# Kernel optimization log

Hardware: AMD Instinct MI355X
Metric: run time of the kernel (lower is better)

The kernel has to match this reference:

```python
import jax, jax.numpy as jnp
import numpy as np

N_USERS, N_RECIPES = 100000, 50000
E, L = 600000, 200000
D_USER, D_RECIPE, H, OUT = 128, 256, 128, 64


def _glorot(key, shape):
    fan_in = shape[-1]
    return jax.random.normal(key, shape, dtype=jnp.float32) / np.sqrt(fan_in)


def setup_inputs() -> dict:
    key = jax.random.key(0)
    ks = jax.random.split(key, 24)
    inp = {
        "x_user": jax.random.normal(ks[0], (N_USERS, D_USER), dtype=jnp.float32),
        "x_recipe": jax.random.normal(ks[1], (N_RECIPES, D_RECIPE), dtype=jnp.float32),
        "edge_src": jax.random.randint(ks[2], (E,), 0, N_USERS, dtype=jnp.int32),
        "edge_dst": jax.random.randint(ks[3], (E,), 0, N_RECIPES, dtype=jnp.int32),
        "lbl_src": jax.random.randint(ks[4], (L,), 0, N_USERS, dtype=jnp.int32),
        "lbl_dst": jax.random.randint(ks[5], (L,), 0, N_RECIPES, dtype=jnp.int32),
        # input projections
        "Wu": _glorot(ks[6], (H, D_USER)), "bu": jnp.zeros((H,), jnp.float32),
        "Wrec": _glorot(ks[7], (H, D_RECIPE)), "brec": jnp.zeros((H,), jnp.float32),
        # conv1: user->recipe and recipe->user SAGEConv (lin_l has bias, lin_r no bias)
        "c1_ur_Wl": _glorot(ks[8], (H, H)), "c1_ur_bl": jnp.zeros((H,), jnp.float32),
        "c1_ur_Wr": _glorot(ks[9], (H, H)),
        "c1_ru_Wl": _glorot(ks[10], (H, H)), "c1_ru_bl": jnp.zeros((H,), jnp.float32),
        "c1_ru_Wr": _glorot(ks[11], (H, H)),
        # conv2
        "c2_ur_Wl": _glorot(ks[12], (OUT, H)), "c2_ur_bl": jnp.zeros((OUT,), jnp.float32),
        "c2_ur_Wr": _glorot(ks[13], (OUT, H)),
        "c2_ru_Wl": _glorot(ks[14], (OUT, H)), "c2_ru_bl": jnp.zeros((OUT,), jnp.float32),
        "c2_ru_Wr": _glorot(ks[15], (OUT, H)),
    }
    return inp


def _sage(x_src, x_dst, src_idx, dst_idx, n_dst, Wl, bl, Wr):
    # gather neighbor features, scatter-mean by destination, then linear + root
    msg = x_src[src_idx]                                    # [E, H]
    agg = jax.ops.segment_sum(msg, dst_idx, num_segments=n_dst)
    cnt = jax.ops.segment_sum(jnp.ones((src_idx.shape[0],), x_src.dtype),
                              dst_idx, num_segments=n_dst)
    mean = agg / jnp.maximum(cnt, 1.0)[:, None]             # nodes w/o edges -> 0
    return mean @ Wl.T + bl + x_dst @ Wr.T


def _forward(x_user, x_recipe, Wu, bu, Wrec, brec,
             c1_ur_Wl, c1_ur_bl, c1_ur_Wr, c1_ru_Wl, c1_ru_bl, c1_ru_Wr,
             c2_ur_Wl, c2_ur_bl, c2_ur_Wr, c2_ru_Wl, c2_ru_bl, c2_ru_Wr,
             edge_src, edge_dst, lbl_src, lbl_dst):
    hu = x_user @ Wu.T + bu           # [N_users, H]
    hr = x_recipe @ Wrec.T + brec     # [N_recipes, H]
    # conv1 (user->recipe updates recipe, recipe->user updates user)
    r1 = jax.nn.relu(_sage(hu, hr, edge_src, edge_dst, hr.shape[0], c1_ur_Wl, c1_ur_bl, c1_ur_Wr))
    u1 = jax.nn.relu(_sage(hr, hu, edge_dst, edge_src, hu.shape[0], c1_ru_Wl, c1_ru_bl, c1_ru_Wr))
    # conv2 (dropout is identity in eval mode)
    zr = _sage(u1, r1, edge_src, edge_dst, r1.shape[0], c2_ur_Wl, c2_ur_bl, c2_ur_Wr)
    zu = _sage(r1, u1, edge_dst, edge_src, u1.shape[0], c2_ru_Wl, c2_ru_bl, c2_ru_Wr)
    # decoder: normalized dot product on labeled user-recipe pairs
    zs = zu[lbl_src]
    zd = zr[lbl_dst]
    zs = zs / jnp.maximum(jnp.linalg.norm(zs, axis=1, keepdims=True), 1e-12)
    zd = zd / jnp.maximum(jnp.linalg.norm(zd, axis=1, keepdims=True), 1e-12)
    return jnp.sum(zs * zd, axis=1)   # [L]


def reference(x_user, x_recipe, edge_src, edge_dst, lbl_src, lbl_dst,
              Wu, bu, Wrec, brec,
              c1_ur_Wl, c1_ur_bl, c1_ur_Wr, c1_ru_Wl, c1_ru_bl, c1_ru_Wr,
              c2_ur_Wl, c2_ur_bl, c2_ur_Wr, c2_ru_Wl, c2_ru_bl, c2_ru_Wr):
    return _forward(x_user, x_recipe, Wu, bu, Wrec, brec,
                    c1_ur_Wl, c1_ur_bl, c1_ur_Wr, c1_ru_Wl, c1_ru_bl, c1_ru_Wr,
                    c2_ur_Wl, c2_ur_bl, c2_ur_Wr, c2_ru_Wl, c2_ru_bl, c2_ru_Wr,
                    edge_src, edge_dst, lbl_src, lbl_dst)
```

## Files before the change

### kernel.cpp

```cpp
#include <hip/hip_runtime.h>
#include <hip/hip_bf16.h>
#include <math.h>

#define N_USERS   100000
#define N_RECIPES 50000
#define NE        600000
#define NL        200000
#define DU        128
#define DR        256
#define H         128
#define OUT_D     64

#define NBKT 256
#define NB_R 196
#define NB_U 391

using half2v = __attribute__((ext_vector_type(2))) _Float16;
using half4v = __attribute__((ext_vector_type(4))) _Float16;
using half8v = __attribute__((ext_vector_type(8))) _Float16;
using f32x4  = __attribute__((ext_vector_type(4))) float;

__device__ __forceinline__ int wave_incl_scan(int v, int lane) {
#pragma unroll
  for (int o = 1; o < 64; o <<= 1) {
    int t = __shfl_up(v, o, 64);
    if (lane >= o) v += t;
  }
  return v;
}

struct WPack {
  const float* src[10];
  _Float16* dst[10];
  int sz4[10];
  int* btot;
};
__global__ void convert_weights(WPack p) {
  const int m = blockIdx.y;
  const int i = blockIdx.x * 256 + threadIdx.x;
  if (m == 0 && blockIdx.x == 0) {
    p.btot[threadIdx.x] = 0;
    p.btot[threadIdx.x + 256] = 0;
  }
  if (i < p.sz4[m]) {
    float4 v = ((const float4*)p.src[m])[i];
    half4v h;
    h[0] = (_Float16)v.x; h[1] = (_Float16)v.y;
    h[2] = (_Float16)v.z; h[3] = (_Float16)v.w;
    ((half4v*)p.dst[m])[i] = h;
  }
}

__global__ __launch_bounds__(256) void csr_phase0(const int* __restrict__ esrc,
                                                  const int* __restrict__ edst,
                                                  int* __restrict__ btot) {
  __shared__ int h[512];
  const int tid = threadIdx.x;
  h[tid] = 0; h[tid + 256] = 0;
  __syncthreads();
  for (int i = blockIdx.x * 256 + tid; i < NE; i += gridDim.x * 256) {
    atomicAdd(&h[edst[i] / NB_R], 1);
    atomicAdd(&h[256 + esrc[i] / NB_U], 1);
  }
  __syncthreads();
  if (h[tid]) atomicAdd(&btot[tid], h[tid]);
  if (h[tid + 256]) atomicAdd(&btot[tid + 256], h[tid + 256]);
}

__global__ void csr_bscan(const int* __restrict__ btot,
                          int* __restrict__ bbase_r, int* __restrict__ bcur_r,
                          int* __restrict__ off_r,
                          int* __restrict__ bbase_u, int* __restrict__ bcur_u,
                          int* __restrict__ off_u) {
  __shared__ int wsum[4];
  const int tid = threadIdx.x, lane = tid & 63, wid = tid >> 6;
#pragma unroll
  for (int dir = 0; dir < 2; ++dir) {
    int v = btot[dir * 256 + tid];
    int inc = wave_incl_scan(v, lane);
    if (lane == 63) wsum[wid] = inc;
    __syncthreads();
    int woff = 0;
#pragma unroll
    for (int w = 0; w < 4; ++w)
      if (w < wid) woff += wsum[w];
    int excl = woff + inc - v;
    int* bbase = dir ? bbase_u : bbase_r;
    int* bcur = dir ? bcur_u : bcur_r;
    bbase[tid] = excl;
    bcur[tid] = excl;
    if (tid == 255) bbase[256] = excl + v;
    __syncthreads();
  }
  if (tid == 0) {
    off_r[N_RECIPES] = NE;
    off_u[N_USERS] = NE;
  }
}

__global__ __launch_bounds__(256) void csr_phase1(
    const int* __restrict__ esrc, const int* __restrict__ edst,
    int* __restrict__ bcur_r, int* __restrict__ bcur_u,
    unsigned* __restrict__ stage_r, unsigned* __restrict__ stage_u) {
  __shared__ int cnt[512];
  __shared__ int gbase[512];
  constexpr int EPT = 8;
  const int BATCH = 256 * EPT;
  const int tid = threadIdx.x;
  for (int base = blockIdx.x * BATCH; base < NE; base += gridDim.x * BATCH) {
    cnt[tid] = 0; cnt[tid + 256] = 0;
    __syncthreads();
    int s_[EPT], d_[EPT], rr_[EPT], ru_[EPT];
#pragma unroll
    for (int e = 0; e < EPT; ++e) {
      const int i = base + e * 256 + tid;
      if (i < NE) {
        const int s = esrc[i], d = edst[i];
        s_[e] = s; d_[e] = d;
        rr_[e] = atomicAdd(&cnt[d / NB_R], 1);
        ru_[e] = atomicAdd(&cnt[256 + s / NB_U], 1);
      } else {
        d_[e] = -1;
      }
    }
    __syncthreads();
    if (cnt[tid]) gbase[tid] = atomicAdd(&bcur_r[tid], cnt[tid]);
    if (cnt[tid + 256]) gbase[tid + 256] = atomicAdd(&bcur_u[tid], cnt[tid + 256]);
    __syncthreads();
#pragma unroll
    for (int e = 0; e < EPT; ++e) {
      if (d_[e] >= 0) {
        const int br = d_[e] / NB_R, lr = d_[e] - br * NB_R;
        stage_r[gbase[br] + rr_[e]] = ((unsigned)lr << 17) | (unsigned)s_[e];
        const int bu = s_[e] / NB_U, lu = s_[e] - bu * NB_U;
        stage_u[gbase[256 + bu] + ru_[e]] = ((unsigned)lu << 17) | (unsigned)d_[e];
      }
    }
    __syncthreads();
  }
}

template <int Nv, int NBv>
__device__ __forceinline__ void phase2_impl(int* cnt, int* wsum,
                                            const unsigned* __restrict__ stage,
                                            const int* __restrict__ bbase,
                                            int* __restrict__ offx,
                                            int* __restrict__ eidx, int B) {
  const int tid = threadIdx.x, lane = tid & 63, wid = tid >> 6;
  const int n0 = B * NBv;
  const int nloc = min(NBv, Nv - n0);
  cnt[tid] = 0; cnt[tid + 256] = 0;
  __syncthreads();
  const int s = bbase[B], e = bbase[B + 1];
  for (int i = s + tid; i < e; i += 256)
    atomicAdd(&cnt[stage[i] >> 17], 1);
  __syncthreads();
  const int e0 = cnt[2 * tid], e1 = cnt[2 * tid + 1];
  const int ssum = e0 + e1;
  int inc = wave_incl_scan(ssum, lane);
  if (lane == 63) wsum[wid] = inc;
  __syncthreads();
  int woff = 0;
#pragma unroll
  for (int w = 0; w < 4; ++w)
    if (w < wid) woff += wsum[w];
  const int base = s + woff + inc - ssum;
  if (2 * tid < nloc) offx[n0 + 2 * tid] = base;
  if (2 * tid + 1 < nloc) offx[n0 + 2 * tid + 1] = base + e0;
  cnt[2 * tid] = base;
  cnt[2 * tid + 1] = base + e0;
  __syncthreads();
  for (int i = s + tid; i < e; i += 256) {
    const unsigned p = stage[i];
    const int pos = atomicAdd(&cnt[p >> 17], 1);
    eidx[pos] = (int)(p & 0x1FFFFu);
  }
}

__global__ __launch_bounds__(256) void csr_phase2(
    const unsigned* __restrict__ stage_r, const int* __restrict__ bbase_r,
    int* __restrict__ off_r, int* __restrict__ eidx_r,
    const unsigned* __restrict__ stage_u, const int* __restrict__ bbase_u,
    int* __restrict__ off_u, int* __restrict__ eidx_u) {
  __shared__ int cnt[512];
  __shared__ int wsum[4];
  if (blockIdx.x < NBKT)
    phase2_impl<N_RECIPES, NB_R>(cnt, wsum, stage_r, bbase_r, off_r, eidx_r, blockIdx.x);
  else
    phase2_impl<N_USERS, NB_U>(cnt, wsum, stage_u, bbase_u, off_u, eidx_u, blockIdx.x - NBKT);
}

template <int ROWH, bool ADD, bool DORELU>
__global__ __launch_bounds__(256) void agg_mean2(
    const _Float16* __restrict__ feat, const int* __restrict__ offx,
    const int* __restrict__ eidx, _Float16* __restrict__ outm, int n_dst) {
  constexpr int L = ROWH / 8;
  const int nid = (int)((blockIdx.x * 256 + threadIdx.x) / L);
  const int ln = threadIdx.x & (L - 1);
  if (nid >= n_dst) return;
  const int s = offx[nid], e = offx[nid + 1];
  float a0[8] = {0}, a1[8] = {0}, a2[8] = {0}, a3[8] = {0};
  int i = s;
  for (; i + 3 < e; i += 4) {
    const int r0 = eidx[i], r1 = eidx[i + 1], r2 = eidx[i + 2], r3 = eidx[i + 3];
    half8v v0 = ((const half8v*)(feat + (size_t)r0 * ROWH))[ln];
    half8v v1 = ((const half8v*)(feat + (size_t)r1 * ROWH))[ln];
    half8v v2 = ((const half8v*)(feat + (size_t)r2 * ROWH))[ln];
    half8v v3 = ((const half8v*)(feat + (size_t)r3 * ROWH))[ln];
#pragma unroll
    for (int t = 0; t < 8; ++t) {
      a0[t] += (float)v0[t];
      a1[t] += (float)v1[t];
      a2[t] += (float)v2[t];
      a3[t] += (float)v3[t];
    }
  }
  for (; i < e; ++i) {
    const int r0 = eidx[i];
    half8v v0 = ((const half8v*)(feat + (size_t)r0 * ROWH))[ln];
#pragma unroll
    for (int t = 0; t < 8; ++t) a0[t] += (float)v0[t];
  }
  const float invc = (e > s) ? 1.f / (float)(e - s) : 0.f;
  half8v o, old;
  if (ADD) old = ((const half8v*)(outm + (size_t)nid * ROWH))[ln];
#pragma unroll
  for (int t = 0; t < 8; ++t) {
    float m = (a0[t] + a1[t] + a2[t] + a3[t]) * invc;
    if (ADD) m += (float)old[t];
    if (DORELU) m = fmaxf(m, 0.f);
    o[t] = (_Float16)m;
  }
  ((half8v*)(outm + (size_t)nid * ROWH))[ln] = o;
}

__global__ __launch_bounds__(256) void agg_mean_dual64(
    const _Float16* __restrict__ fA, const int* __restrict__ offA,
    const int* __restrict__ eA, _Float16* __restrict__ oA,
    const _Float16* __restrict__ fB, const int* __restrict__ offB,
    const int* __restrict__ eB, _Float16* __restrict__ oB) {
  const int gnid = (int)((blockIdx.x * 256 + threadIdx.x) >> 3);
  const int ln = threadIdx.x & 7;
  if (gnid >= N_RECIPES + N_USERS) return;
  const _Float16* feat;
  const int* offx;
  const int* eidx;
  _Float16* outm;
  int nid;
  if (gnid < N_RECIPES) {
    feat = fA; offx = offA; eidx = eA; outm = oA; nid = gnid;
  } else {
    feat = fB; offx = offB; eidx = eB; outm = oB; nid = gnid - N_RECIPES;
  }
  const int s = offx[nid], e = offx[nid + 1];
  float a0[8] = {0}, a1[8] = {0}, a2[8] = {0}, a3[8] = {0};
  int i = s;
  for (; i + 3 < e; i += 4) {
    const int r0 = eidx[i], r1 = eidx[i + 1], r2 = eidx[i + 2], r3 = eidx[i + 3];
    half8v v0 = ((const half8v*)(feat + (size_t)r0 * OUT_D))[ln];
    half8v v1 = ((const half8v*)(feat + (size_t)r1 * OUT_D))[ln];
    half8v v2 = ((const half8v*)(feat + (size_t)r2 * OUT_D))[ln];
    half8v v3 = ((const half8v*)(feat + (size_t)r3 * OUT_D))[ln];
#pragma unroll
    for (int t = 0; t < 8; ++t) {
      a0[t] += (float)v0[t];
      a1[t] += (float)v1[t];
      a2[t] += (float)v2[t];
      a3[t] += (float)v3[t];
    }
  }
  for (; i < e; ++i) {
    const int r0 = eidx[i];
    half8v v0 = ((const half8v*)(feat + (size_t)r0 * OUT_D))[ln];
#pragma unroll
    for (int t = 0; t < 8; ++t) a0[t] += (float)v0[t];
  }
  const float invc = (e > s) ? 1.f / (float)(e - s) : 0.f;
  half8v old = ((const half8v*)(outm + (size_t)nid * OUT_D))[ln];
  half8v o;
#pragma unroll
  for (int t = 0; t < 8; ++t)
    o[t] = (_Float16)((a0[t] + a1[t] + a2[t] + a3[t]) * invc + (float)old[t]);
  ((half8v*)(outm + (size_t)nid * OUT_D))[ln] = o;
}

template <int BN, int K, bool DUAL, bool BIAS, bool RELU, bool A_F32>
__global__ __launch_bounds__(256) void gemm_direct(
    const void* __restrict__ A1v, const _Float16* __restrict__ W1,
    const void* __restrict__ A2v, const _Float16* __restrict__ W2,
    const float* __restrict__ bias, _Float16* __restrict__ outp, int M) {
  constexpr int WN = BN / 64;
  constexpr int BM = (4 / WN) * 64;
  const int lane = threadIdx.x & 63;
  const int wid = threadIdx.x >> 6;
  const int wm = wid / WN;
  const int wn = wid % WN;
  const int m0 = blockIdx.x * BM;
  const int lm = lane & 15;
  const int lkb = (lane >> 4) * 8;

  f32x4 acc[4][4];
  const f32x4 zero4 = {0.f, 0.f, 0.f, 0.f};
#pragma unroll
  for (int i = 0; i < 4; ++i)
#pragma unroll
    for (int j = 0; j < 4; ++j) acc[i][j] = zero4;

  int arow[4];
#pragma unroll
  for (int i = 0; i < 4; ++i) {
    int r = m0 + wm * 64 + i * 16 + lm;
    arow[i] = (r < M) ? r : (M - 1);
  }

#pragma unroll
  for (int pass = 0; pass < (DUAL ? 2 : 1); ++pass) {
    const void* Av = pass ? A2v : A1v;
    const _Float16* __restrict__ W = pass ? W2 : W1;
#pragma unroll
    for (int k0 = 0; k0 < K; k0 += 32) {
      half8v af[4], bf[4];
      if constexpr (A_F32) {
        const float* __restrict__ A = (const float*)Av;
#pragma unroll
        for (int i = 0; i < 4; ++i) {
          const float* p = A + (size_t)arow[i] * K + k0 + lkb;
          float4 u = *(const float4*)p;
          float4 v = *(const float4*)(p + 4);
          af[i][0] = (_Float16)u.x; af[i][1] = (_Float16)u.y;
          af[i][2] = (_Float16)u.z; af[i][3] = (_Float16)u.w;
          af[i][4] = (_Float16)v.x; af[i][5] = (_Float16)v.y;
          af[i][6] = (_Float16)v.z; af[i][7] = (_Float16)v.w;
        }
      } else {
        const _Float16* __restrict__ A = (const _Float16*)Av;
#pragma unroll
        for (int i = 0; i < 4; ++i)
          af[i] = *(const half8v*)(A + (size_t)arow[i] * K + k0 + lkb);
      }
#pragma unroll
      for (int j = 0; j < 4; ++j)
        bf[j] = *(const half8v*)(W + (size_t)(wn * 64 + j * 16 + lm) * K + k0 + lkb);
#pragma unroll
      for (int i = 0; i < 4; ++i)
#pragma unroll
        for (int j = 0; j < 4; ++j)
          acc[i][j] = __builtin_amdgcn_mfma_f32_16x16x32_f16(af[i], bf[j], acc[i][j], 0, 0, 0);
    }
  }
  const int rb = (lane >> 4) * 4;
#pragma unroll
  for (int j = 0; j < 4; ++j) {
    const int col = wn * 64 + j * 16 + lm;
    float bj = 0.f;
    if constexpr (BIAS) bj = bias[col];
#pragma unroll
    for (int i = 0; i < 4; ++i) {
#pragma unroll
      for (int r = 0; r < 4; ++r) {
        const int grow = m0 + wm * 64 + i * 16 + rb + r;
        if (grow < M) {
          float v = acc[i][j][r] + bj;
          if (RELU) v = fmaxf(v, 0.f);
          outp[(size_t)grow * BN + col] = (_Float16)v;
        }
      }
    }
  }
}

struct GParts {
  const void* A[4];
  const _Float16* W[4];
  const float* bias[4];
  _Float16* out[4];
  int M[4];
  int K[4];
  int blk0[4];
};

template <int BN, bool A_F32>
__global__ __launch_bounds__(256) void gemm_parts(GParts P) {
  constexpr int WN = BN / 64;
  constexpr int BM = (4 / WN) * 64;
  const int bid = blockIdx.x;
  const int p = (bid >= P.blk0[1]) + (bid >= P.blk0[2]) + (bid >= P.blk0[3]);
  const int K = P.K[p];
  const int M = P.M[p];
  const int m0 = (bid - P.blk0[p]) * BM;
  const _Float16* __restrict__ W = P.W[p];
  const float* __restrict__ bias = P.bias[p];
  _Float16* __restrict__ outp = P.out[p];

  const int lane = threadIdx.x & 63;
  const int wid = threadIdx.x >> 6;
  const int wm = wid / WN;
  const int wn = wid % WN;
  const int lm = lane & 15;
  const int lkb = (lane >> 4) * 8;

  f32x4 acc[4][4];
  const f32x4 zero4 = {0.f, 0.f, 0.f, 0.f};
#pragma unroll
  for (int i = 0; i < 4; ++i)
#pragma unroll
    for (int j = 0; j < 4; ++j) acc[i][j] = zero4;

  int arow[4];
#pragma unroll
  for (int i = 0; i < 4; ++i) {
    int r = m0 + wm * 64 + i * 16 + lm;
    arow[i] = (r < M) ? r : (M - 1);
  }

  if constexpr (A_F32) {
    const float* ap[4];
    const _Float16* wp_[4];
#pragma unroll
    for (int i = 0; i < 4; ++i) ap[i] = (const float*)P.A[p] + (size_t)arow[i] * K + lkb;
#pragma unroll
    for (int j = 0; j < 4; ++j) wp_[j] = W + (size_t)(wn * 64 + j * 16 + lm) * K + lkb;
    for (int k0 = 0; k0 < K; k0 += 32) {
      half8v af[4], bf[4];
#pragma unroll
      for (int i = 0; i < 4; ++i) {
        float4 u = *(const float4*)ap[i];
        float4 v = *(const float4*)(ap[i] + 4);
        af[i][0] = (_Float16)u.x; af[i][1] = (_Float16)u.y;
        af[i][2] = (_Float16)u.z; af[i][3] = (_Float16)u.w;
        af[i][4] = (_Float16)v.x; af[i][5] = (_Float16)v.y;
        af[i][6] = (_Float16)v.z; af[i][7] = (_Float16)v.w;
        ap[i] += 32;
      }
#pragma unroll
      for (int j = 0; j < 4; ++j) {
        bf[j] = *(const half8v*)wp_[j];
        wp_[j] += 32;
      }
#pragma unroll
      for (int i = 0; i < 4; ++i)
#pragma unroll
        for (int j = 0; j < 4; ++j)
          acc[i][j] = __builtin_amdgcn_mfma_f32_16x16x32_f16(af[i], bf[j], acc[i][j], 0, 0, 0);
    }
  } else {
    const _Float16* ap[4];
    const _Float16* wp_[4];
#pragma unroll
    for (int i = 0; i < 4; ++i) ap[i] = (const _Float16*)P.A[p] + (size_t)arow[i] * K + lkb;
#pragma unroll
    for (int j = 0; j < 4; ++j) wp_[j] = W + (size_t)(wn * 64 + j * 16 + lm) * K + lkb;
    for (int k0 = 0; k0 < K; k0 += 32) {
      half8v af[4], bf[4];
#pragma unroll
      for (int i = 0; i < 4; ++i) {
        af[i] = *(const half8v*)ap[i];
        ap[i] += 32;
      }
#pragma unroll
      for (int j = 0; j < 4; ++j) {
        bf[j] = *(const half8v*)wp_[j];
        wp_[j] += 32;
      }
#pragma unroll
      for (int i = 0; i < 4; ++i)
#pragma unroll
        for (int j = 0; j < 4; ++j)
          acc[i][j] = __builtin_amdgcn_mfma_f32_16x16x32_f16(af[i], bf[j], acc[i][j], 0, 0, 0);
    }
  }

  const int rb = (lane >> 4) * 4;
#pragma unroll
  for (int j = 0; j < 4; ++j) {
    const int col = wn * 64 + j * 16 + lm;
    const float bj = bias ? bias[col] : 0.f;
#pragma unroll
    for (int i = 0; i < 4; ++i) {
#pragma unroll
      for (int r = 0; r < 4; ++r) {
        const int grow = m0 + wm * 64 + i * 16 + rb + r;
        if (grow < M)
          outp[(size_t)grow * BN + col] = (_Float16)(acc[i][j][r] + bj);
      }
    }
  }
}

__global__ __launch_bounds__(256) void decoder_f16(
    const _Float16* __restrict__ zu, const _Float16* __restrict__ zr,
    const int* __restrict__ ls, const int* __restrict__ ld,
    float* __restrict__ outp) {
  const int w = (blockIdx.x * 256 + threadIdx.x) >> 6;
  if (w >= NL) return;
  const int lane = threadIdx.x & 63;
  const int hl = lane & 31;
  const _Float16* src = (lane >= 32) ? (zr + (size_t)ld[w] * OUT_D)
                                     : (zu + (size_t)ls[w] * OUT_D);
  half2v v = ((const half2v*)src)[hl];
  float x0 = (float)v[0], x1 = (float)v[1];
  float y0 = __shfl_xor(x0, 32, 64);
  float y1 = __shfl_xor(x1, 32, 64);
  float nx = x0 * x0 + x1 * x1;
  float ny = y0 * y0 + y1 * y1;
  float ab = x0 * y0 + x1 * y1;
#pragma unroll
  for (int o = 16; o > 0; o >>= 1) {
    nx += __shfl_xor(nx, o, 64);
    ny += __shfl_xor(ny, o, 64);
    ab += __shfl_xor(ab, o, 64);
  }
  if (lane == 0) {
    float denom = fmaxf(sqrtf(nx), 1e-12f) * fmaxf(sqrtf(ny), 1e-12f);
    outp[w] = ab / denom;
  }
}

extern "C" void kernel_launch(void* const* d_in, const int* in_sizes, int n_in,
                              void* d_out, int out_size, void* d_ws, size_t ws_size,
                              hipStream_t stream) {
  (void)in_sizes; (void)n_in; (void)out_size; (void)ws_size;
  const float* x_user   = (const float*)d_in[0];
  const float* x_recipe = (const float*)d_in[1];
  const int* edge_src   = (const int*)d_in[2];
  const int* edge_dst   = (const int*)d_in[3];
  const int* lbl_src    = (const int*)d_in[4];
  const int* lbl_dst    = (const int*)d_in[5];
  const float* Wu       = (const float*)d_in[6];
  const float* bu       = (const float*)d_in[7];
  const float* Wrec     = (const float*)d_in[8];
  const float* brec     = (const float*)d_in[9];
  const float* c1_ur_Wl = (const float*)d_in[10];
  const float* c1_ur_bl = (const float*)d_in[11];
  const float* c1_ur_Wr = (const float*)d_in[12];
  const float* c1_ru_Wl = (const float*)d_in[13];
  const float* c1_ru_bl = (const float*)d_in[14];
  const float* c1_ru_Wr = (const float*)d_in[15];
  const float* c2_ur_Wl = (const float*)d_in[16];
  const float* c2_ur_bl = (const float*)d_in[17];
  const float* c2_ur_Wr = (const float*)d_in[18];
  const float* c2_ru_Wl = (const float*)d_in[19];
  const float* c2_ru_bl = (const float*)d_in[20];
  const float* c2_ru_Wr = (const float*)d_in[21];
  float* out = (float*)d_out;

  char* ws = (char*)d_ws;
  size_t off = 0;
  auto take = [&](size_t bytes) -> void* {
    void* p = ws + off;
    off = (off + bytes + 255) & ~(size_t)255;
    return p;
  };
  _Float16* hu    = (_Float16*)take((size_t)N_USERS * H * 2);
  _Float16* hr    = (_Float16*)take((size_t)N_RECIPES * H * 2);
  _Float16* meanr = (_Float16*)take((size_t)N_RECIPES * H * 2);
  _Float16* r1    = (_Float16*)take((size_t)N_RECIPES * H * 2);
  _Float16* u1    = (_Float16*)take((size_t)N_USERS * H * 2);
  int* off_r  = (int*)take((size_t)(N_RECIPES + 1) * 4);
  int* off_u  = (int*)take((size_t)(N_USERS + 1) * 4);
  int* eidx_r = (int*)take((size_t)NE * 4);
  int* eidx_u = (int*)take((size_t)NE * 4);
  unsigned* stage_r = (unsigned*)take((size_t)NE * 4);
  unsigned* stage_u = (unsigned*)take((size_t)NE * 4);
  int* btot    = (int*)take(512 * 4);
  int* bbase_r = (int*)take(257 * 4);
  int* bbase_u = (int*)take(257 * 4);
  int* bcur_r  = (int*)take(256 * 4);
  int* bcur_u  = (int*)take(256 * 4);
  _Float16* Wu_h     = (_Float16*)take(H * DU * 2);
  _Float16* Wrec_h   = (_Float16*)take(H * DR * 2);
  _Float16* c1urWl_h = (_Float16*)take(H * H * 2);
  _Float16* c1urWr_h = (_Float16*)take(H * H * 2);
  _Float16* c1ruWl_h = (_Float16*)take(H * H * 2);
  _Float16* c1ruWr_h = (_Float16*)take(H * H * 2);
  _Float16* c2urWl_h = (_Float16*)take(OUT_D * H * 2);
  _Float16* c2urWr_h = (_Float16*)take(OUT_D * H * 2);
  _Float16* c2ruWl_h = (_Float16*)take(OUT_D * H * 2);
  _Float16* c2ruWr_h = (_Float16*)take(OUT_D * H * 2);
  _Float16* t_r1 = meanr;
  _Float16* t_u2 = hr;
  _Float16* t_r2 = meanr;
  _Float16* zr   = hu;
  _Float16* zu   = hu + (size_t)N_RECIPES * OUT_D;

  WPack wp;
  wp.src[0] = Wu;       wp.dst[0] = Wu_h;      wp.sz4[0] = H * DU / 4;
  wp.src[1] = Wrec;     wp.dst[1] = Wrec_h;    wp.sz4[1] = H * DR / 4;
  wp.src[2] = c1_ur_Wl; wp.dst[2] = c1urWl_h;  wp.sz4[2] = H * H / 4;
  wp.src[3] = c1_ur_Wr; wp.dst[3] = c1urWr_h;  wp.sz4[3] = H * H / 4;
  wp.src[4] = c1_ru_Wl; wp.dst[4] = c1ruWl_h;  wp.sz4[4] = H * H / 4;
  wp.src[5] = c1_ru_Wr; wp.dst[5] = c1ruWr_h;  wp.sz4[5] = H * H / 4;
  wp.src[6] = c2_ur_Wl; wp.dst[6] = c2urWl_h;  wp.sz4[6] = OUT_D * H / 4;
  wp.src[7] = c2_ur_Wr; wp.dst[7] = c2urWr_h;  wp.sz4[7] = OUT_D * H / 4;
  wp.src[8] = c2_ru_Wl; wp.dst[8] = c2ruWl_h;  wp.sz4[8] = OUT_D * H / 4;
  wp.src[9] = c2_ru_Wr; wp.dst[9] = c2ruWr_h;  wp.sz4[9] = OUT_D * H / 4;
  wp.btot = btot;
  convert_weights<<<dim3(32, 10), 256, 0, stream>>>(wp);

  csr_phase0<<<512, 256, 0, stream>>>(edge_src, edge_dst, btot);
  csr_bscan<<<1, 256, 0, stream>>>(btot, bbase_r, bcur_r, off_r, bbase_u, bcur_u, off_u);
  csr_phase1<<<(NE + 2047) / 2048, 256, 0, stream>>>(edge_src, edge_dst, bcur_r, bcur_u,
                                                     stage_r, stage_u);
  csr_phase2<<<2 * NBKT, 256, 0, stream>>>(stage_r, bbase_r, off_r, eidx_r,
                                           stage_u, bbase_u, off_u, eidx_u);

  {
    GParts P;
    P.A[0] = x_user;   P.W[0] = Wu_h;   P.bias[0] = bu;   P.out[0] = hu;
    P.M[0] = N_USERS;  P.K[0] = DU;     P.blk0[0] = 0;
    P.A[1] = x_recipe; P.W[1] = Wrec_h; P.bias[1] = brec; P.out[1] = hr;
    P.M[1] = N_RECIPES; P.K[1] = DR;    P.blk0[1] = 782;
    P.A[2] = P.A[3] = nullptr; P.W[2] = P.W[3] = nullptr;
    P.bias[2] = P.bias[3] = nullptr; P.out[2] = P.out[3] = nullptr;
    P.M[2] = P.M[3] = 1; P.K[2] = P.K[3] = 32;
    P.blk0[2] = P.blk0[3] = 0x7fffffff;
    gemm_parts<128, true><<<782 + 391, 256, 0, stream>>>(P);
  }

  agg_mean2<H, false, false><<<(N_RECIPES * 16 + 255) / 256, 256, 0, stream>>>(
      hu, off_r, eidx_r, meanr, N_RECIPES);
  gemm_direct<128, H, true, true, true, false><<<(N_RECIPES + 127) / 128, 256, 0, stream>>>(
      meanr, c1urWl_h, hr, c1urWr_h, c1_ur_bl, r1, N_RECIPES);
  {
    GParts P;
    P.A[0] = hr; P.W[0] = c1ruWl_h; P.bias[0] = nullptr;  P.out[0] = t_r1;
    P.M[0] = N_RECIPES; P.K[0] = H; P.blk0[0] = 0;
    P.A[1] = hu; P.W[1] = c1ruWr_h; P.bias[1] = c1_ru_bl; P.out[1] = u1;
    P.M[1] = N_USERS;   P.K[1] = H; P.blk0[1] = 391;
    P.A[2] = P.A[3] = nullptr; P.W[2] = P.W[3] = nullptr;
    P.bias[2] = P.bias[3] = nullptr; P.out[2] = P.out[3] = nullptr;
    P.M[2] = P.M[3] = 1; P.K[2] = P.K[3] = 32;
    P.blk0[2] = P.blk0[3] = 0x7fffffff;
    gemm_parts<128, false><<<391 + 782, 256, 0, stream>>>(P);
  }
  agg_mean2<H, true, true><<<(N_USERS * 16 + 255) / 256, 256, 0, stream>>>(
      t_r1, off_u, eidx_u, u1, N_USERS);

  {
    GParts P;
    P.A[0] = u1; P.W[0] = c2urWl_h; P.bias[0] = nullptr;  P.out[0] = t_u2;
    P.M[0] = N_USERS;   P.K[0] = H; P.blk0[0] = 0;
    P.A[1] = r1; P.W[1] = c2urWr_h; P.bias[1] = c2_ur_bl; P.out[1] = zr;
    P.M[1] = N_RECIPES; P.K[1] = H; P.blk0[1] = 391;
    P.A[2] = r1; P.W[2] = c2ruWl_h; P.bias[2] = nullptr;  P.out[2] = t_r2;
    P.M[2] = N_RECIPES; P.K[2] = H; P.blk0[2] = 587;
    P.A[3] = u1; P.W[3] = c2ruWr_h; P.bias[3] = c2_ru_bl; P.out[3] = zu;
    P.M[3] = N_USERS;   P.K[3] = H; P.blk0[3] = 783;
    gemm_parts<64, false><<<391 + 196 + 196 + 391, 256, 0, stream>>>(P);
  }
  agg_mean_dual64<<<((N_RECIPES + N_USERS) * 8 + 255) / 256, 256, 0, stream>>>(
      t_u2, off_r, eidx_r, zr, t_r2, off_u, eidx_u, zu);

  decoder_f16<<<((size_t)NL * 64 + 255) / 256, 256, 0, stream>>>(zu, zr, lbl_src, lbl_dst, out);
}
```

Measured before the change: 498.9 us.

## Pre-convert inputs to fp16, merge conv1 GEMMs into one grouped launch

Result: slower. 511.9 us (+2.6%).

```diff
diff --git a/kernel.cpp b/kernel.cpp
--- a/kernel.cpp
+++ b/kernel.cpp
@@ -29,25 +29,27 @@
   return v;
 }
 
-struct WPack {
-  const float* src[10];
-  _Float16* dst[10];
-  int sz4[10];
+struct CPack {
+  const float* src[12];
+  _Float16* dst[12];
+  int n4[12];
   int* btot;
 };
-__global__ void convert_weights(WPack p) {
+__global__ __launch_bounds__(256) void convert_all(CPack p) {
   const int m = blockIdx.y;
-  const int i = blockIdx.x * 256 + threadIdx.x;
   if (m == 0 && blockIdx.x == 0) {
     p.btot[threadIdx.x] = 0;
     p.btot[threadIdx.x + 256] = 0;
   }
-  if (i < p.sz4[m]) {
-    float4 v = ((const float4*)p.src[m])[i];
+  const int n = p.n4[m];
+  const float4* __restrict__ s = (const float4*)p.src[m];
+  half4v* __restrict__ d = (half4v*)p.dst[m];
+  for (int i = blockIdx.x * 256 + threadIdx.x; i < n; i += gridDim.x * 256) {
+    float4 v = s[i];
     half4v h;
     h[0] = (_Float16)v.x; h[1] = (_Float16)v.y;
     h[2] = (_Float16)v.z; h[3] = (_Float16)v.w;
-    ((half4v*)p.dst[m])[i] = h;
+    d[i] = h;
   }
 }
 
@@ -284,114 +286,55 @@
   ((half8v*)(outm + (size_t)nid * OUT_D))[ln] = o;
 }
 
-template <int BN, int K, bool DUAL, bool BIAS, bool RELU, bool A_F32>
-__global__ __launch_bounds__(256) void gemm_direct(
-    const void* __restrict__ A1v, const _Float16* __restrict__ W1,
-    const void* __restrict__ A2v, const _Float16* __restrict__ W2,
-    const float* __restrict__ bias, _Float16* __restrict__ outp, int M) {
-  constexpr int WN = BN / 64;
-  constexpr int BM = (4 / WN) * 64;
-  const int lane = threadIdx.x & 63;
-  const int wid = threadIdx.x >> 6;
-  const int wm = wid / WN;
-  const int wn = wid % WN;
-  const int m0 = blockIdx.x * BM;
-  const int lm = lane & 15;
-  const int lkb = (lane >> 4) * 8;
-
-  f32x4 acc[4][4];
-  const f32x4 zero4 = {0.f, 0.f, 0.f, 0.f};
-#pragma unroll
-  for (int i = 0; i < 4; ++i)
-#pragma unroll
-    for (int j = 0; j < 4; ++j) acc[i][j] = zero4;
-
-  int arow[4];
-#pragma unroll
-  for (int i = 0; i < 4; ++i) {
-    int r = m0 + wm * 64 + i * 16 + lm;
-    arow[i] = (r < M) ? r : (M - 1);
-  }
-
-#pragma unroll
-  for (int pass = 0; pass < (DUAL ? 2 : 1); ++pass) {
-    const void* Av = pass ? A2v : A1v;
-    const _Float16* __restrict__ W = pass ? W2 : W1;
-#pragma unroll
-    for (int k0 = 0; k0 < K; k0 += 32) {
-      half8v af[4], bf[4];
-      if constexpr (A_F32) {
-        const float* __restrict__ A = (const float*)Av;
-#pragma unroll
-        for (int i = 0; i < 4; ++i) {
-          const float* p = A + (size_t)arow[i] * K + k0 + lkb;
-          float4 u = *(const float4*)p;
-          float4 v = *(const float4*)(p + 4);
-          af[i][0] = (_Float16)u.x; af[i][1] = (_Float16)u.y;
-          af[i][2] = (_Float16)u.z; af[i][3] = (_Float16)u.w;
-          af[i][4] = (_Float16)v.x; af[i][5] = (_Float16)v.y;
-          af[i][6] = (_Float16)v.z; af[i][7] = (_Float16)v.w;
-        }
-      } else {
-        const _Float16* __restrict__ A = (const _Float16*)Av;
-#pragma unroll
-        for (int i = 0; i < 4; ++i)
-          af[i] = *(const half8v*)(A + (size_t)arow[i] * K + k0 + lkb);
-      }
-#pragma unroll
-      for (int j = 0; j < 4; ++j)
-        bf[j] = *(const half8v*)(W + (size_t)(wn * 64 + j * 16 + lm) * K + k0 + lkb);
-#pragma unroll
-      for (int i = 0; i < 4; ++i)
-#pragma unroll
-        for (int j = 0; j < 4; ++j)
-          acc[i][j] = __builtin_amdgcn_mfma_f32_16x16x32_f16(af[i], bf[j], acc[i][j], 0, 0, 0);
-    }
-  }
-  const int rb = (lane >> 4) * 4;
-#pragma unroll
-  for (int j = 0; j < 4; ++j) {
-    const int col = wn * 64 + j * 16 + lm;
-    float bj = 0.f;
-    if constexpr (BIAS) bj = bias[col];
-#pragma unroll
-    for (int i = 0; i < 4; ++i) {
-#pragma unroll
-      for (int r = 0; r < 4; ++r) {
-        const int grow = m0 + wm * 64 + i * 16 + rb + r;
-        if (grow < M) {
-          float v = acc[i][j][r] + bj;
-          if (RELU) v = fmaxf(v, 0.f);
-          outp[(size_t)grow * BN + col] = (_Float16)v;
-        }
-      }
-    }
-  }
-}
-
 struct GParts {
-  const void* A[4];
-  const _Float16* W[4];
+  const _Float16* A1[4];
+  const _Float16* W1[4];
+  const _Float16* A2[4];
+  const _Float16* W2[4];
   const float* bias[4];
   _Float16* out[4];
   int M[4];
-  int K[4];
+  int np1[4];
+  int np2[4];
+  int relu[4];
   int blk0[4];
 };
 
-template <int BN, bool A_F32>
+__device__ __forceinline__ void gemm_accum_k128(
+    const _Float16* __restrict__ A, const _Float16* __restrict__ W, int np,
+    const int arow[4], const int wrow[4], int lkb, f32x4 (&acc)[4][4]) {
+  const int Kt = np << 7;
+  for (int kp = 0; kp < np; ++kp) {
+    half8v af[4][4], bf[4][4];
+#pragma unroll
+    for (int ks = 0; ks < 4; ++ks) {
+      const int ko = (kp << 7) + ks * 32 + lkb;
+#pragma unroll
+      for (int i = 0; i < 4; ++i)
+        af[ks][i] = *(const half8v*)(A + (size_t)arow[i] * Kt + ko);
+#pragma unroll
+      for (int j = 0; j < 4; ++j)
+        bf[ks][j] = *(const half8v*)(W + (size_t)wrow[j] * Kt + ko);
+    }
+#pragma unroll
+    for (int ks = 0; ks < 4; ++ks)
+#pragma unroll
+      for (int i = 0; i < 4; ++i)
+#pragma unroll
+        for (int j = 0; j < 4; ++j)
+          acc[i][j] = __builtin_amdgcn_mfma_f32_16x16x32_f16(af[ks][i], bf[ks][j],
+                                                             acc[i][j], 0, 0, 0);
+  }
+}
+
+template <int BN>
 __global__ __launch_bounds__(256) void gemm_parts(GParts P) {
   constexpr int WN = BN / 64;
   constexpr int BM = (4 / WN) * 64;
   const int bid = blockIdx.x;
   const int p = (bid >= P.blk0[1]) + (bid >= P.blk0[2]) + (bid >= P.blk0[3]);
-  const int K = P.K[p];
   const int M = P.M[p];
   const int m0 = (bid - P.blk0[p]) * BM;
-  const _Float16* __restrict__ W = P.W[p];
-  const float* __restrict__ bias = P.bias[p];
-  _Float16* __restrict__ outp = P.out[p];
-
   const int lane = threadIdx.x & 63;
   const int wid = threadIdx.x >> 6;
   const int wm = wid / WN;
@@ -399,89 +342,45 @@
   const int lm = lane & 15;
   const int lkb = (lane >> 4) * 8;
 
-  f32x4 acc[4][4];
-  const f32x4 zero4 = {0.f, 0.f, 0.f, 0.f};
-#pragma unroll
-  for (int i = 0; i < 4; ++i)
-#pragma unroll
-    for (int j = 0; j < 4; ++j) acc[i][j] = zero4;
-
   int arow[4];
 #pragma unroll
   for (int i = 0; i < 4; ++i) {
     int r = m0 + wm * 64 + i * 16 + lm;
     arow[i] = (r < M) ? r : (M - 1);
   }
-
-  if constexpr (A_F32) {
-    const float* ap[4];
-    const _Float16* wp_[4];
-#pragma unroll
-    for (int i = 0; i < 4; ++i) ap[i] = (const float*)P.A[p] + (size_t)arow[i] * K + lkb;
-#pragma unroll
-    for (int j = 0; j < 4; ++j) wp_[j] = W + (size_t)(wn * 64 + j * 16 + lm) * K + lkb;
-    for (int k0 = 0; k0 < K; k0 += 32) {
-      half8v af[4], bf[4];
-#pragma unroll
-      for (int i = 0; i < 4; ++i) {
-        float4 u = *(const float4*)ap[i];
-        float4 v = *(const float4*)(ap[i] + 4);
-        af[i][0] = (_Float16)u.x; af[i][1] = (_Float16)u.y;
-        af[i][2] = (_Float16)u.z; af[i][3] = (_Float16)u.w;
-        af[i][4] = (_Float16)v.x; af[i][5] = (_Float16)v.y;
-        af[i][6] = (_Float16)v.z; af[i][7] = (_Float16)v.w;
-        ap[i] += 32;
-      }
-#pragma unroll
-      for (int j = 0; j < 4; ++j) {
-        bf[j] = *(const half8v*)wp_[j];
-        wp_[j] += 32;
-      }
-#pragma unroll
-      for (int i = 0; i < 4; ++i)
-#pragma unroll
-        for (int j = 0; j < 4; ++j)
-          acc[i][j] = __builtin_amdgcn_mfma_f32_16x16x32_f16(af[i], bf[j], acc[i][j], 0, 0, 0);
-    }
-  } else {
-    const _Float16* ap[4];
-    const _Float16* wp_[4];
-#pragma unroll
-    for (int i = 0; i < 4; ++i) ap[i] = (const _Float16*)P.A[p] + (size_t)arow[i] * K + lkb;
-#pragma unroll
-    for (int j = 0; j < 4; ++j) wp_[j] = W + (size_t)(wn * 64 + j * 16 + lm) * K + lkb;
-    for (int k0 = 0; k0 < K; k0 += 32) {
-      half8v af[4], bf[4];
-#pragma unroll
-      for (int i = 0; i < 4; ++i) {
-        af[i] = *(const half8v*)ap[i];
-        ap[i] += 32;
-      }
-#pragma unroll
-      for (int j = 0; j < 4; ++j) {
-        bf[j] = *(const half8v*)wp_[j];
-        wp_[j] += 32;
-      }
-#pragma unroll
-      for (int i = 0; i < 4; ++i)
-#pragma unroll
-        for (int j = 0; j < 4; ++j)
-          acc[i][j] = __builtin_amdgcn_mfma_f32_16x16x32_f16(af[i], bf[j], acc[i][j], 0, 0, 0);
-    }
-  }
-
+  int wrow[4];
+#pragma unroll
+  for (int j = 0; j < 4; ++j) wrow[j] = wn * 64 + j * 16 + lm;
+
+  f32x4 acc[4][4];
+  const f32x4 zero4 = {0.f, 0.f, 0.f, 0.f};
+#pragma unroll
+  for (int i = 0; i < 4; ++i)
+#pragma unroll
+    for (int j = 0; j < 4; ++j) acc[i][j] = zero4;
+
+  gemm_accum_k128(P.A1[p], P.W1[p], P.np1[p], arow, wrow, lkb, acc);
+  const int np2 = P.np2[p];
+  if (np2 > 0) gemm_accum_k128(P.A2[p], P.W2[p], np2, arow, wrow, lkb, acc);
+
+  const float* __restrict__ bias = P.bias[p];
+  const int dorelu = P.relu[p];
+  _Float16* __restrict__ outp = P.out[p];
   const int rb = (lane >> 4) * 4;
 #pragma unroll
   for (int j = 0; j < 4; ++j) {
-    const int col = wn * 64 + j * 16 + lm;
+    const int col = wrow[j];
     const float bj = bias ? bias[col] : 0.f;
 #pragma unroll
     for (int i = 0; i < 4; ++i) {
 #pragma unroll
       for (int r = 0; r < 4; ++r) {
         const int grow = m0 + wm * 64 + i * 16 + rb + r;
-        if (grow < M)
-          outp[(size_t)grow * BN + col] = (_Float16)(acc[i][j][r] + bj);
+        if (grow < M) {
+          float v = acc[i][j][r] + bj;
+          if (dorelu) v = fmaxf(v, 0.f);
+          outp[(size_t)grow * BN + col] = (_Float16)v;
+        }
       }
     }
   }
@@ -556,6 +455,9 @@
   _Float16* meanr = (_Float16*)take((size_t)N_RECIPES * H * 2);
   _Float16* r1    = (_Float16*)take((size_t)N_RECIPES * H * 2);
   _Float16* u1    = (_Float16*)take((size_t)N_USERS * H * 2);
+  _Float16* t_r1  = (_Float16*)take((size_t)N_RECIPES * H * 2);
+  _Float16* xu_h  = (_Float16*)take((size_t)N_USERS * DU * 2);
+  _Float16* xr_h  = (_Float16*)take((size_t)N_RECIPES * DR * 2);
   int* off_r  = (int*)take((size_t)(N_RECIPES + 1) * 4);
   int* off_u  = (int*)take((size_t)(N_USERS + 1) * 4);
   int* eidx_r = (int*)take((size_t)NE * 4);
@@ -577,25 +479,26 @@
   _Float16* c2urWr_h = (_Float16*)take(OUT_D * H * 2);
   _Float16* c2ruWl_h = (_Float16*)take(OUT_D * H * 2);
   _Float16* c2ruWr_h = (_Float16*)take(OUT_D * H * 2);
-  _Float16* t_r1 = meanr;
   _Float16* t_u2 = hr;
   _Float16* t_r2 = meanr;
   _Float16* zr   = hu;
   _Float16* zu   = hu + (size_t)N_RECIPES * OUT_D;
 
-  WPack wp;
-  wp.src[0] = Wu;       wp.dst[0] = Wu_h;      wp.sz4[0] = H * DU / 4;
-  wp.src[1] = Wrec;     wp.dst[1] = Wrec_h;    wp.sz4[1] = H * DR / 4;
-  wp.src[2] = c1_ur_Wl; wp.dst[2] = c1urWl_h;  wp.sz4[2] = H * H / 4;
-  wp.src[3] = c1_ur_Wr; wp.dst[3] = c1urWr_h;  wp.sz4[3] = H * H / 4;
-  wp.src[4] = c1_ru_Wl; wp.dst[4] = c1ruWl_h;  wp.sz4[4] = H * H / 4;
-  wp.src[5] = c1_ru_Wr; wp.dst[5] = c1ruWr_h;  wp.sz4[5] = H * H / 4;
-  wp.src[6] = c2_ur_Wl; wp.dst[6] = c2urWl_h;  wp.sz4[6] = OUT_D * H / 4;
-  wp.src[7] = c2_ur_Wr; wp.dst[7] = c2urWr_h;  wp.sz4[7] = OUT_D * H / 4;
-  wp.src[8] = c2_ru_Wl; wp.dst[8] = c2ruWl_h;  wp.sz4[8] = OUT_D * H / 4;
-  wp.src[9] = c2_ru_Wr; wp.dst[9] = c2ruWr_h;  wp.sz4[9] = OUT_D * H / 4;
-  wp.btot = btot;
-  convert_weights<<<dim3(32, 10), 256, 0, stream>>>(wp);
+  CPack cp;
+  cp.src[0] = x_user;   cp.dst[0] = xu_h;      cp.n4[0] = N_USERS * DU / 4;
+  cp.src[1] = x_recipe; cp.dst[1] = xr_h;      cp.n4[1] = N_RECIPES * DR / 4;
+  cp.src[2] = Wu;       cp.dst[2] = Wu_h;      cp.n4[2] = H * DU / 4;
+  cp.src[3] = Wrec;     cp.dst[3] = Wrec_h;    cp.n4[3] = H * DR / 4;
+  cp.src[4] = c1_ur_Wl; cp.dst[4] = c1urWl_h;  cp.n4[4] = H * H / 4;
+  cp.src[5] = c1_ur_Wr; cp.dst[5] = c1urWr_h;  cp.n4[5] = H * H / 4;
+  cp.src[6] = c1_ru_Wl; cp.dst[6] = c1ruWl_h;  cp.n4[6] = H * H / 4;
+  cp.src[7] = c1_ru_Wr; cp.dst[7] = c1ruWr_h;  cp.n4[7] = H * H / 4;
+  cp.src[8] = c2_ur_Wl; cp.dst[8] = c2urWl_h;  cp.n4[8] = OUT_D * H / 4;
+  cp.src[9] = c2_ur_Wr; cp.dst[9] = c2urWr_h;  cp.n4[9] = OUT_D * H / 4;
+  cp.src[10] = c2_ru_Wl; cp.dst[10] = c2ruWl_h; cp.n4[10] = OUT_D * H / 4;
+  cp.src[11] = c2_ru_Wr; cp.dst[11] = c2ruWr_h; cp.n4[11] = OUT_D * H / 4;
+  cp.btot = btot;
+  convert_all<<<dim3(512, 12), 256, 0, stream>>>(cp);
 
   csr_phase0<<<512, 256, 0, stream>>>(edge_src, edge_dst, btot);
   csr_bscan<<<1, 256, 0, stream>>>(btot, bbase_r, bcur_r, off_r, bbase_u, bcur_u, off_u);
@@ -604,49 +507,62 @@
   csr_phase2<<<2 * NBKT, 256, 0, stream>>>(stage_r, bbase_r, off_r, eidx_r,
                                            stage_u, bbase_u, off_u, eidx_u);
 
+  auto clear_parts = [](GParts& P, int from) {
+    for (int q = from; q < 4; ++q) {
+      P.A1[q] = P.A2[q] = nullptr; P.W1[q] = P.W2[q] = nullptr;
+      P.bias[q] = nullptr; P.out[q] = nullptr;
+      P.M[q] = 1; P.np1[q] = 0; P.np2[q] = 0; P.relu[q] = 0;
+      P.blk0[q] = 0x7fffffff;
+    }
+  };
+
   {
     GParts P;
-    P.A[0] = x_user;   P.W[0] = Wu_h;   P.bias[0] = bu;   P.out[0] = hu;
-    P.M[0] = N_USERS;  P.K[0] = DU;     P.blk0[0] = 0;
-    P.A[1] = x_recipe; P.W[1] = Wrec_h; P.bias[1] = brec; P.out[1] = hr;
-    P.M[1] = N_RECIPES; P.K[1] = DR;    P.blk0[1] = 782;
-    P.A[2] = P.A[3] = nullptr; P.W[2] = P.W[3] = nullptr;
-    P.bias[2] = P.bias[3] = nullptr; P.out[2] = P.out[3] = nullptr;
-    P.M[2] = P.M[3] = 1; P.K[2] = P.K[3] = 32;
-    P.blk0[2] = P.blk0[3] = 0x7fffffff;
-    gemm_parts<128, true><<<782 + 391, 256, 0, stream>>>(P);
+    P.A1[0] = xu_h; P.W1[0] = Wu_h;   P.A2[0] = nullptr; P.W2[0] = nullptr;
+    P.bias[0] = bu;   P.out[0] = hu; P.M[0] = N_USERS;   P.np1[0] = 1; P.np2[0] = 0;
+    P.relu[0] = 0; P.blk0[0] = 0;
+    P.A1[1] = xr_h; P.W1[1] = Wrec_h; P.A2[1] = nullptr; P.W2[1] = nullptr;
+    P.bias[1] = brec; P.out[1] = hr; P.M[1] = N_RECIPES; P.np1[1] = 2; P.np2[1] = 0;
+    P.relu[1] = 0; P.blk0[1] = 782;
+    clear_parts(P, 2);
+    gemm_parts<128><<<782 + 391, 256, 0, stream>>>(P);
   }
 
   agg_mean2<H, false, false><<<(N_RECIPES * 16 + 255) / 256, 256, 0, stream>>>(
       hu, off_r, eidx_r, meanr, N_RECIPES);
-  gemm_direct<128, H, true, true, true, false><<<(N_RECIPES + 127) / 128, 256, 0, stream>>>(
-      meanr, c1urWl_h, hr, c1urWr_h, c1_ur_bl, r1, N_RECIPES);
+
   {
     GParts P;
-    P.A[0] = hr; P.W[0] = c1ruWl_h; P.bias[0] = nullptr;  P.out[0] = t_r1;
-    P.M[0] = N_RECIPES; P.K[0] = H; P.blk0[0] = 0;
-    P.A[1] = hu; P.W[1] = c1ruWr_h; P.bias[1] = c1_ru_bl; P.out[1] = u1;
-    P.M[1] = N_USERS;   P.K[1] = H; P.blk0[1] = 391;
-    P.A[2] = P.A[3] = nullptr; P.W[2] = P.W[3] = nullptr;
-    P.bias[2] = P.bias[3] = nullptr; P.out[2] = P.out[3] = nullptr;
-    P.M[2] = P.M[3] = 1; P.K[2] = P.K[3] = 32;
-    P.blk0[2] = P.blk0[3] = 0x7fffffff;
-    gemm_parts<128, false><<<391 + 782, 256, 0, stream>>>(P);
+    P.A1[0] = meanr; P.W1[0] = c1urWl_h; P.A2[0] = hr; P.W2[0] = c1urWr_h;
+    P.bias[0] = c1_ur_bl; P.out[0] = r1; P.M[0] = N_RECIPES;
+    P.np1[0] = 1; P.np2[0] = 1; P.relu[0] = 1; P.blk0[0] = 0;
+    P.A1[1] = hr; P.W1[1] = c1ruWl_h; P.A2[1] = nullptr; P.W2[1] = nullptr;
+    P.bias[1] = nullptr; P.out[1] = t_r1; P.M[1] = N_RECIPES;
+    P.np1[1] = 1; P.np2[1] = 0; P.relu[1] = 0; P.blk0[1] = 391;
+    P.A1[2] = hu; P.W1[2] = c1ruWr_h; P.A2[2] = nullptr; P.W2[2] = nullptr;
+    P.bias[2] = c1_ru_bl; P.out[2] = u1; P.M[2] = N_USERS;
+    P.np1[2] = 1; P.np2[2] = 0; P.relu[2] = 0; P.blk0[2] = 782;
+    clear_parts(P, 3);
+    gemm_parts<128><<<391 + 391 + 782, 256, 0, stream>>>(P);
   }
   agg_mean2<H, true, true><<<(N_USERS * 16 + 255) / 256, 256, 0, stream>>>(
       t_r1, off_u, eidx_u, u1, N_USERS);
 
   {
     GParts P;
-    P.A[0] = u1; P.W[0] = c2urWl_h; P.bias[0] = nullptr;  P.out[0] = t_u2;
-    P.M[0] = N_USERS;   P.K[0] = H; P.blk0[0] = 0;
-    P.A[1] = r1; P.W[1] = c2urWr_h; P.bias[1] = c2_ur_bl; P.out[1] = zr;
-    P.M[1] = N_RECIPES; P.K[1] = H; P.blk0[1] = 391;
-    P.A[2] = r1; P.W[2] = c2ruWl_h; P.bias[2] = nullptr;  P.out[2] = t_r2;
-    P.M[2] = N_RECIPES; P.K[2] = H; P.blk0[2] = 587;
-    P.A[3] = u1; P.W[3] = c2ruWr_h; P.bias[3] = c2_ru_bl; P.out[3] = zu;
-    P.M[3] = N_USERS;   P.K[3] = H; P.blk0[3] = 783;
-    gemm_parts<64, false><<<391 + 196 + 196 + 391, 256, 0, stream>>>(P);
+    P.A1[0] = u1; P.W1[0] = c2urWl_h; P.bias[0] = nullptr;  P.out[0] = t_u2;
+    P.M[0] = N_USERS;   P.blk0[0] = 0;
+    P.A1[1] = r1; P.W1[1] = c2urWr_h; P.bias[1] = c2_ur_bl; P.out[1] = zr;
+    P.M[1] = N_RECIPES; P.blk0[1] = 391;
+    P.A1[2] = r1; P.W1[2] = c2ruWl_h; P.bias[2] = nullptr;  P.out[2] = t_r2;
+    P.M[2] = N_RECIPES; P.blk0[2] = 587;
+    P.A1[3] = u1; P.W1[3] = c2ruWr_h; P.bias[3] = c2_ru_bl; P.out[3] = zu;
+    P.M[3] = N_USERS;   P.blk0[3] = 783;
+    for (int q = 0; q < 4; ++q) {
+      P.A2[q] = nullptr; P.W2[q] = nullptr;
+      P.np1[q] = 1; P.np2[q] = 0; P.relu[q] = 0;
+    }
+    gemm_parts<64><<<391 + 196 + 196 + 391, 256, 0, stream>>>(P);
   }
   agg_mean_dual64<<<((N_RECIPES + N_USERS) * 8 + 255) / 256, 256, 0, stream>>>(
       t_u2, off_r, eidx_r, zr, t_r2, off_u, eidx_u, zu);
```
